# Optimization experiments

Measured on AMD Instinct MI355X. Metric: run time of the kernel, lower is better.

Reference implementation:

```python
import jax, jax.numpy as jnp
import numpy as np

N_USERS = 100_000
N_ITEMS = 100_000
D = 64
B = 16_384
L_U = 50   # items per user history
N_F = 32   # friends per user
L_I = 50   # users per item history


def setup_inputs() -> dict:
    key = jax.random.key(0)
    ks = jax.random.split(key, 22)
    s = 0.1  # xavier-ish scale for D=64
    return {
        "user_ids": jax.random.randint(ks[0], (B,), 0, N_USERS),
        "item_ids": jax.random.randint(ks[1], (B,), 0, N_ITEMS),
        "user_hist_items": jax.random.randint(ks[2], (B, L_U), 0, N_ITEMS),
        "user_hist_ratings": jax.random.uniform(ks[3], (B, L_U), jnp.float32, 1.0, 5.0),
        "user_friends": jax.random.randint(ks[4], (B, N_F), 0, N_USERS),
        "item_hist_users": jax.random.randint(ks[5], (B, L_I), 0, N_USERS),
        "item_hist_ratings": jax.random.uniform(ks[6], (B, L_I), jnp.float32, 1.0, 5.0),
        "embed_user": jax.random.normal(ks[7], (N_USERS, D), jnp.float32) * s,
        "embed_item": jax.random.normal(ks[8], (N_ITEMS, D), jnp.float32) * s,
        "W1": jax.random.normal(ks[9], (D, D), jnp.float32) * s,
        "W2": jax.random.normal(ks[10], (D, D), jnp.float32) * s,
        "W3": jax.random.normal(ks[11], (D, 1), jnp.float32) * s,
        "W4": jax.random.normal(ks[12], (D, D), jnp.float32) * s,
        "W5": jax.random.normal(ks[13], (D, D), jnp.float32) * s,
        "W6": jax.random.normal(ks[14], (D, 1), jnp.float32) * s,
        "W7": jax.random.normal(ks[15], (D, D), jnp.float32) * s,
        "W8": jax.random.normal(ks[16], (D, D), jnp.float32) * s,
        "W9": jax.random.normal(ks[17], (D, 1), jnp.float32) * s,
        "fc1_w": jax.random.normal(ks[18], (2 * D, D), jnp.float32) * s,
        "fc1_b": jnp.zeros((D,), jnp.float32),
        "fc2_w": jax.random.normal(ks[19], (D, 1), jnp.float32) * s,
        "fc2_b": jnp.zeros((1,), jnp.float32),
    }


def _attention(q_emb, neigh, Wq, Wk, Wa, ratings=None):
    # q_emb: [B, D]; neigh: [B, L, D]; ratings: [B, L] or None
    a = q_emb @ Wq  # [B, D]
    a = a[:, None, :] + neigh @ Wk  # [B, L, D]
    if ratings is not None:
        a = a + ratings[..., None] * neigh
    w = jax.nn.softmax((a @ Wa)[..., 0], axis=1)  # [B, L]
    return jnp.einsum("bl,bld->bd", w, neigh)


def reference(user_ids, item_ids, user_hist_items, user_hist_ratings,
              user_friends, item_hist_users, item_hist_ratings,
              embed_user, embed_item,
              W1, W2, W3, W4, W5, W6, W7, W8, W9,
              fc1_w, fc1_b, fc2_w, fc2_b):
    user_emb = embed_user[user_ids]          # [B, D]
    item_emb = embed_item[item_ids]          # [B, D]

    # user <- rated items attention (W1, W2, W3)
    hist_item_embs = embed_item[user_hist_items]        # [B, L_U, D]
    user_items_emb = _attention(user_emb, hist_item_embs, W1, W2, W3,
                                user_hist_ratings)

    # user <- friends attention (W4, W5, W6)
    friend_embs = embed_user[user_friends]               # [B, N_F, D]
    user_social_emb = _attention(user_emb, friend_embs, W4, W5, W6)

    user_emb_final = user_emb + user_items_emb + user_social_emb

    # item <- interacting users attention (W7, W8, W9)
    hist_user_embs = embed_user[item_hist_users]         # [B, L_I, D]
    item_users_emb = _attention(item_emb, hist_user_embs, W7, W8, W9,
                                item_hist_ratings)
    item_emb_final = item_emb + item_users_emb

    concat = jnp.concatenate([user_emb_final, item_emb_final], axis=1)  # [B, 2D]
    h = jax.nn.relu(concat @ fc1_w + fc1_b)
    out = (h @ fc2_w + fc2_b)[:, 0]  # [B]
    return out
```

## Files before the change

kernel.cpp:

```cpp
#include <hip/hip_runtime.h>
#include <hip/hip_bf16.h>
#include <math.h>

#define B_TOTAL 16384
#define D 64
#define L_U 50
#define N_F 32
#define L_I 50
#define ROWOFF(l) (((l) << 6) + ((((l) >> 1)) << 2))
#define TILE_FL 3296

__global__ void graphrec_setup(const float* __restrict__ W1, const float* __restrict__ W2,
                               const float* __restrict__ W3, const float* __restrict__ W4,
                               const float* __restrict__ W5, const float* __restrict__ W6,
                               const float* __restrict__ W7, const float* __restrict__ W8,
                               const float* __restrict__ W9, float* __restrict__ u) {
    int t = threadIdx.x;
    int w = t >> 6;
    int d = t & 63;
    const float* Wm;
    const float* Wv;
    switch (w) {
        case 0: Wm = W1; Wv = W3; break;
        case 1: Wm = W2; Wv = W3; break;
        case 2: Wm = W4; Wv = W6; break;
        case 3: Wm = W5; Wv = W6; break;
        case 4: Wm = W7; Wv = W9; break;
        default: Wm = W8; Wv = W9; break;
    }
    float s = 0.f;
    #pragma unroll
    for (int j = 0; j < D; ++j) s = fmaf(Wm[d * D + j], Wv[j], s);
    u[w * D + d] = s;
}

__device__ __forceinline__ float wred_sum(float x) {
    float t;
    #define STEP_ADD(ctrl, rmask)                                                        \
        t = __int_as_float(__builtin_amdgcn_update_dpp(0, __float_as_int(x),             \
                                                       ctrl, rmask, 0xf, false));        \
        x = x + t;
    STEP_ADD(0x111, 0xf)
    STEP_ADD(0x112, 0xf)
    STEP_ADD(0x114, 0xf)
    STEP_ADD(0x118, 0xf)
    STEP_ADD(0x142, 0xa)
    STEP_ADD(0x143, 0xc)
    #undef STEP_ADD
    return __int_as_float(__builtin_amdgcn_readlane(__float_as_int(x), 63));
}
__device__ __forceinline__ float wred_max(float x) {
    const int NEG_INF = 0xFF800000;
    float t;
    #define STEP_MAX(ctrl, rmask)                                                        \
        t = __int_as_float(__builtin_amdgcn_update_dpp(NEG_INF, __float_as_int(x),       \
                                                       ctrl, rmask, 0xf, false));        \
        x = fmaxf(x, t);
    STEP_MAX(0x111, 0xf)
    STEP_MAX(0x112, 0xf)
    STEP_MAX(0x114, 0xf)
    STEP_MAX(0x118, 0xf)
    STEP_MAX(0x142, 0xa)
    STEP_MAX(0x143, 0xc)
    #undef STEP_MAX
    return __int_as_float(__builtin_amdgcn_readlane(__float_as_int(x), 63));
}

template <int L, bool HAS_R>
__device__ __forceinline__ float attn3(float cq, const float* __restrict__ table,
                                       const float4* __restrict__ u2g,
                                       const float4* __restrict__ wag,
                                       int idxreg, float r, int lane, float* tile) {
    asm volatile("s_waitcnt lgkmcnt(0)" ::: "memory");

    #pragma unroll
    for (int l = 0; l < L; ++l) {
        int idx = __builtin_amdgcn_readlane(idxreg, l);
        const float* gp = table + (size_t)(unsigned)idx * D + lane;
        __builtin_amdgcn_global_load_lds(
            (const __attribute__((address_space(1))) void*)gp,
            (__attribute__((address_space(3))) void*)(tile + ROWOFF(l)),
            4, 0, 0);
    }
    asm volatile("s_waitcnt vmcnt(0)" ::: "memory");

    const int rl = (lane < L) ? lane : (L - 1);
    const float* row = tile + ROWOFF(rl);
    float dotU = 0.f, dotW = 0.f;
    #pragma unroll
    for (int j = 0; j < D / 4; ++j) {
        float4 n = *(const float4*)(row + 4 * j);
        float4 uu = u2g[j];
        dotU = fmaf(n.x, uu.x, fmaf(n.y, uu.y, fmaf(n.z, uu.z, fmaf(n.w, uu.w, dotU))));
        if (HAS_R) {
            float4 ww = wag[j];
            dotW = fmaf(n.x, ww.x, fmaf(n.y, ww.y, fmaf(n.z, ww.z, fmaf(n.w, ww.w, dotW))));
        }
    }
    float sc = cq + dotU;
    if (HAS_R) sc = fmaf(r, dotW, sc);
    sc = (lane < L) ? sc : -1e30f;

    float m = wred_max(sc);
    float e = __expf(sc - m);
    float s = wred_sum(e);
    float w = e * (1.0f / s);

    float acc = 0.f;
    #pragma unroll
    for (int l = 0; l < L; ++l) {
        float wl = __int_as_float(__builtin_amdgcn_readlane(__float_as_int(w), l));
        acc = fmaf(wl, tile[ROWOFF(l) + lane], acc);
    }
    return acc;
}

__global__ __launch_bounds__(256) void graphrec_fwd(
        const int* __restrict__ user_ids, const int* __restrict__ item_ids,
        const int* __restrict__ uh_items, const float* __restrict__ uh_rat,
        const int* __restrict__ ufriends,
        const int* __restrict__ ih_users, const float* __restrict__ ih_rat,
        const float* __restrict__ eu, const float* __restrict__ ei,
        const float* __restrict__ W3, const float* __restrict__ W6,
        const float* __restrict__ W9,
        const float* __restrict__ fc1w, const float* __restrict__ fc1b,
        const float* __restrict__ fc2w, const float* __restrict__ fc2b,
        const float* __restrict__ u, float* __restrict__ out) {
    __shared__ __align__(16) float smem[4 * TILE_FL];
    const int lane = threadIdx.x & 63;
    const int wv = threadIdx.x >> 6;
    const int b = blockIdx.x * 4 + wv;
    float* tile = smem + wv * TILE_FL;

    int idxA = 0, idxB = 0, idxC = 0;
    float rA = 0.f, rC = 0.f;
    if (lane < L_U) {
        idxA = uh_items[b * L_U + lane];
        rA   = uh_rat[b * L_U + lane];
        idxC = ih_users[b * L_I + lane];
        rC   = ih_rat[b * L_I + lane];
    }
    if (lane < N_F) idxB = ufriends[b * N_F + lane];

    const int uid = user_ids[b];
    const int iid = item_ids[b];
    const float qu = eu[(size_t)uid * D + lane];
    const float qi = ei[(size_t)iid * D + lane];

    const float cqa = wred_sum(qu * u[lane]);
    const float cqb = wred_sum(qu * u[128 + lane]);
    const float cqc = wred_sum(qi * u[256 + lane]);

    const float accA = attn3<L_U, true >(cqa, ei, (const float4*)(u + 64),
                                         (const float4*)W3, idxA, rA, lane, tile);
    const float accB = attn3<N_F, false>(cqb, eu, (const float4*)(u + 192),
                                         (const float4*)W6, idxB, 0.f, lane, tile);
    const float accC = attn3<L_I, true >(cqc, eu, (const float4*)(u + 320),
                                         (const float4*)W9, idxC, rC, lane, tile);

    const float uf  = qu + accA + accB;
    const float itf = qi + accC;

    float h = fc1b[lane];
    #pragma unroll
    for (int k = 0; k < D; ++k) {
        float c = __int_as_float(__builtin_amdgcn_readlane(__float_as_int(uf), k));
        h = fmaf(c, fc1w[k * D + lane], h);
    }
    #pragma unroll
    for (int k = 0; k < D; ++k) {
        float c = __int_as_float(__builtin_amdgcn_readlane(__float_as_int(itf), k));
        h = fmaf(c, fc1w[(D + k) * D + lane], h);
    }
    h = fmaxf(h, 0.f);
    float o = wred_sum(h * fc2w[lane]);
    if (lane == 0) out[b] = o + fc2b[0];
}

extern "C" void kernel_launch(void* const* d_in, const int* in_sizes, int n_in,
                              void* d_out, int out_size, void* d_ws, size_t ws_size,
                              hipStream_t stream) {
    const int*   user_ids = (const int*)d_in[0];
    const int*   item_ids = (const int*)d_in[1];
    const int*   uh_items = (const int*)d_in[2];
    const float* uh_rat   = (const float*)d_in[3];
    const int*   ufriends = (const int*)d_in[4];
    const int*   ih_users = (const int*)d_in[5];
    const float* ih_rat   = (const float*)d_in[6];
    const float* eu       = (const float*)d_in[7];
    const float* ei       = (const float*)d_in[8];
    const float* W1 = (const float*)d_in[9];
    const float* W2 = (const float*)d_in[10];
    const float* W3 = (const float*)d_in[11];
    const float* W4 = (const float*)d_in[12];
    const float* W5 = (const float*)d_in[13];
    const float* W6 = (const float*)d_in[14];
    const float* W7 = (const float*)d_in[15];
    const float* W8 = (const float*)d_in[16];
    const float* W9 = (const float*)d_in[17];
    const float* fc1w = (const float*)d_in[18];
    const float* fc1b = (const float*)d_in[19];
    const float* fc2w = (const float*)d_in[20];
    const float* fc2b = (const float*)d_in[21];
    float* out = (float*)d_out;
    float* u   = (float*)d_ws;

    graphrec_setup<<<1, 384, 0, stream>>>(W1, W2, W3, W4, W5, W6, W7, W8, W9, u);
    graphrec_fwd<<<B_TOTAL / 4, 256, 0, stream>>>(
        user_ids, item_ids, uh_items, uh_rat, ufriends, ih_users, ih_rat,
        eu, ei, W3, W6, W9, fc1w, fc1b, fc2w, fc2b, u, out);
}
```

Measured before the change: 210.0 us.

## Prefetch neighbor embedding rows into registers and overlap gathers with attention

Replaces the per-row dword global-to-LDS gathers with float4 loads into registers. Each quarter-wave fetches one neighbor row, with the row index broadcast via ds_bpermute. The item-history and friend gathers are issued early, and the third gather is issued before the first attention computes, so memory latency overlaps softmax and weighted-sum work. Row padding changes to one pad per 4 rows to match the new write pattern, and launch bounds request 3 blocks per CU. The cost is much higher register pressure from the staged buffers, with a risk of spills or reduced occupancy.

```diff
diff --git a/kernel.cpp b/kernel.cpp
--- a/kernel.cpp
+++ b/kernel.cpp
@@ -7,8 +7,8 @@
 #define L_U 50
 #define N_F 32
 #define L_I 50
-#define ROWOFF(l) (((l) << 6) + ((((l) >> 1)) << 2))
-#define TILE_FL 3296
+#define ROWOFF(l) (((l) << 6) + ((((l) >> 2)) << 2))
+#define TILE_FL 3248
 
 __global__ void graphrec_setup(const float* __restrict__ W1, const float* __restrict__ W2,
                                const float* __restrict__ W3, const float* __restrict__ W4,
@@ -66,24 +66,37 @@
     return __int_as_float(__builtin_amdgcn_readlane(__float_as_int(x), 63));
 }
 
+template <int L>
+__device__ __forceinline__ void stage_load(const float* __restrict__ table,
+                                           int idxreg, int lane, float4* buf) {
+    const int sub = lane >> 4;
+    const int co = (lane & 15) << 2;
+    #pragma unroll
+    for (int g = 0; g < (L + 3) / 4; ++g) {
+        int l = 4 * g + sub;
+        if (l > L - 1) l = L - 1;
+        int ridx = __builtin_amdgcn_ds_bpermute(l << 2, idxreg);
+        buf[g] = *(const float4*)(table + (size_t)(unsigned)ridx * D + co);
+    }
+}
+
+template <int L>
+__device__ __forceinline__ void stage_write(const float4* buf, int lane, float* tile) {
+    const int sub = lane >> 4;
+    const int co = (lane & 15) << 2;
+    #pragma unroll
+    for (int g = 0; g < (L + 3) / 4; ++g) {
+        int l = 4 * g + sub;
+        if (l > L - 1) l = L - 1;
+        *(float4*)(tile + (l << 6) + (g << 2) + co) = buf[g];
+    }
+}
+
 template <int L, bool HAS_R>
-__device__ __forceinline__ float attn3(float cq, const float* __restrict__ table,
-                                       const float4* __restrict__ u2g,
-                                       const float4* __restrict__ wag,
-                                       int idxreg, float r, int lane, float* tile) {
-    asm volatile("s_waitcnt lgkmcnt(0)" ::: "memory");
-
-    #pragma unroll
-    for (int l = 0; l < L; ++l) {
-        int idx = __builtin_amdgcn_readlane(idxreg, l);
-        const float* gp = table + (size_t)(unsigned)idx * D + lane;
-        __builtin_amdgcn_global_load_lds(
-            (const __attribute__((address_space(1))) void*)gp,
-            (__attribute__((address_space(3))) void*)(tile + ROWOFF(l)),
-            4, 0, 0);
-    }
-    asm volatile("s_waitcnt vmcnt(0)" ::: "memory");
-
+__device__ __forceinline__ float attn_compute(float cq,
+                                              const float4* __restrict__ u2g,
+                                              const float4* __restrict__ wag,
+                                              float r, int lane, const float* tile) {
     const int rl = (lane < L) ? lane : (L - 1);
     const float* row = tile + ROWOFF(rl);
     float dotU = 0.f, dotW = 0.f;
@@ -115,7 +128,7 @@
     return acc;
 }
 
-__global__ __launch_bounds__(256) void graphrec_fwd(
+__global__ __launch_bounds__(256, 3) void graphrec_fwd(
         const int* __restrict__ user_ids, const int* __restrict__ item_ids,
         const int* __restrict__ uh_items, const float* __restrict__ uh_rat,
         const int* __restrict__ ufriends,
@@ -142,6 +155,11 @@
     }
     if (lane < N_F) idxB = ufriends[b * N_F + lane];
 
+    float4 bufA[(L_U + 3) / 4];
+    float4 bufB[(N_F + 3) / 4];
+    stage_load<L_U>(ei, idxA, lane, bufA);
+    stage_load<N_F>(eu, idxB, lane, bufB);
+
     const int uid = user_ids[b];
     const int iid = item_ids[b];
     const float qu = eu[(size_t)uid * D + lane];
@@ -151,12 +169,19 @@
     const float cqb = wred_sum(qu * u[128 + lane]);
     const float cqc = wred_sum(qi * u[256 + lane]);
 
-    const float accA = attn3<L_U, true >(cqa, ei, (const float4*)(u + 64),
-                                         (const float4*)W3, idxA, rA, lane, tile);
-    const float accB = attn3<N_F, false>(cqb, eu, (const float4*)(u + 192),
-                                         (const float4*)W6, idxB, 0.f, lane, tile);
-    const float accC = attn3<L_I, true >(cqc, eu, (const float4*)(u + 320),
-                                         (const float4*)W9, idxC, rC, lane, tile);
+    stage_write<L_U>(bufA, lane, tile);
+    float4 bufC[(L_I + 3) / 4];
+    stage_load<L_I>(eu, idxC, lane, bufC);
+    const float accA = attn_compute<L_U, true >(cqa, (const float4*)(u + 64),
+                                                (const float4*)W3, rA, lane, tile);
+
+    stage_write<N_F>(bufB, lane, tile);
+    const float accB = attn_compute<N_F, false>(cqb, (const float4*)(u + 192),
+                                                (const float4*)W6, 0.f, lane, tile);
+
+    stage_write<L_I>(bufC, lane, tile);
+    const float accC = attn_compute<L_I, true >(cqc, (const float4*)(u + 320),
+                                                (const float4*)W9, rC, lane, tile);
 
     const float uf  = qu + accA + accB;
     const float itf = qi + accC;
```

After: 205.1 us. -2.3%, faster.
